# Kernel optimization log

Hardware: AMD Instinct MI355X
Metric: run time of the kernel (lower is better)

The kernel has to match this reference:

```python
import jax, jax.numpy as jnp
import numpy as np

L, B, D = 2048, 8, 2048


def setup_inputs() -> dict:
    key = jax.random.key(0)
    k1, k2, k3 = jax.random.split(key, 3)
    x = jax.random.normal(k1, (L, B, D), dtype=jnp.float32)
    x_mix_last = jnp.zeros((B, D), dtype=jnp.float32)
    factor_param = jax.random.uniform(k2, (D,), dtype=jnp.float32)
    W = jax.random.normal(k3, (D, D), dtype=jnp.float32) * (1.0 / np.sqrt(D))
    return {"x": x, "x_mix_last": x_mix_last, "factor_param": factor_param, "W": W}


def reference(x, x_mix_last, factor_param, W):
    seq_len = x.shape[0]
    factor = jax.nn.sigmoid(factor_param)                      # [D]
    t = jnp.arange(seq_len, dtype=x.dtype)[:, None]            # [L,1]
    factor_progression = jnp.power(factor[None, :], t)         # [L,D] = factor**t
    # FFT-based causal convolution: y[t] = sum_{s<=t} factor**(t-s) * x[s]
    n = 2 * seq_len
    fft_fp = jnp.fft.rfft(factor_progression, n=n, axis=0)     # [L+1, D]
    fft_x = jnp.fft.rfft(x, n=n, axis=0)                       # [L+1, B, D]
    conv = jnp.fft.irfft(fft_x * fft_fp[:, None, :], axis=0)[:seq_len]  # [L,B,D]
    conv = conv.astype(x.dtype)
    # EMA mix: carried state decays as factor**(t+1); new input weighted by (1-factor)
    x_mix = (x_mix_last[None, :, :] * factor_progression[:, None, :] * factor
             + (1.0 - factor) * conv)                          # [L,B,D]
    # Linear mixing W (no bias): out = x_mix @ W.T
    return jnp.einsum('lbd,ed->lbe', x_mix, W)
```

## Files before the change

### kernel.cpp

```cpp
#include <hip/hip_runtime.h>
#include <hip/hip_bf16.h>
#include <stdint.h>

#define L_SEQ 2048
#define BATCH 8
#define DIM   2048
#define M_DIM (L_SEQ * BATCH)
#define N_DIM DIM
#define K_DIM DIM

typedef short bf16x8 __attribute__((ext_vector_type(8)));
typedef float f32x4  __attribute__((ext_vector_type(4)));
typedef unsigned short u16x4 __attribute__((ext_vector_type(4)));

__device__ inline unsigned short f2bf_rn(float f) {
    unsigned int u = __float_as_uint(f);
    u += 0x7FFF + ((u >> 16) & 1);
    return (unsigned short)(u >> 16);
}

__device__ inline void gload16(const void* g, void* l) {
    __builtin_amdgcn_global_load_lds(
        (const __attribute__((address_space(1))) void*)g,
        (__attribute__((address_space(3))) void*)l, 16, 0, 0);
}

__global__ void cvt_w_kernel(const float* __restrict__ W,
                             unsigned short* __restrict__ Wb) {
    int i = blockIdx.x * 256 + threadIdx.x;
    const float4 v = *reinterpret_cast<const float4*>(W + (size_t)i * 4);
    u16x4 r;
    r.x = f2bf_rn(v.x); r.y = f2bf_rn(v.y);
    r.z = f2bf_rn(v.z); r.w = f2bf_rn(v.w);
    *reinterpret_cast<u16x4*>(Wb + (size_t)i * 4) = r;
}

#define SCH 128
#define SLB 64
__global__ void ema_scan_kernel(const float* __restrict__ x,
                                const float* __restrict__ xml,
                                const float* __restrict__ fparam,
                                unsigned short* __restrict__ xm) {
    int g  = blockIdx.x * 256 + threadIdx.x;
    int dp = (g & 1023) * 2;
    int b  = (g >> 10) & (BATCH - 1);
    int ch = g >> 13;

    float2 pv = *reinterpret_cast<const float2*>(fparam + dp);
    const float f0 = 1.0f / (1.0f + expf(-pv.x));
    const float f1 = 1.0f / (1.0f + expf(-pv.y));
    float2 xlv = *reinterpret_cast<const float2*>(xml + b * DIM + dp);
    const float om0 = 1.0f - f0, om1 = 1.0f - f1;

    const int t0 = ch * SCH;
    int ts = t0 - SLB; if (ts < 0) ts = 0;
    const int stride2 = (BATCH * DIM) / 2;

    const float2* xp = reinterpret_cast<const float2*>(x) +
                       (size_t)ts * stride2 + (b * DIM + dp) / 2;
    float c0 = 0.0f, c1 = 0.0f;
    #pragma unroll 8
    for (int t = ts; t < t0; ++t) {
        float2 v = *xp;
        c0 = fmaf(c0, f0, v.x);
        c1 = fmaf(c1, f1, v.y);
        xp += stride2;
    }
    float pw0 = powf(f0, (float)(t0 + 1));
    float pw1 = powf(f1, (float)(t0 + 1));
    ushort2* op = reinterpret_cast<ushort2*>(xm + (size_t)t0 * BATCH * DIM + b * DIM + dp);
    #pragma unroll 8
    for (int k = 0; k < SCH; ++k) {
        float2 v = *xp;
        c0 = fmaf(c0, f0, v.x);
        c1 = fmaf(c1, f1, v.y);
        ushort2 r;
        r.x = f2bf_rn(fmaf(xlv.x, pw0, om0 * c0));
        r.y = f2bf_rn(fmaf(xlv.y, pw1, om1 * c1));
        *op = r;
        pw0 *= f0; pw1 *= f1;
        xp += stride2; op += stride2;
    }
}

#define NT_K (K_DIM / 64)
#define NI   (NT_K / 2)

__global__ void __launch_bounds__(512, 2)
gemm8_kernel(const unsigned short* __restrict__ A,
             const unsigned short* __restrict__ Bt,
             float* __restrict__ C) {
    extern __shared__ __attribute__((aligned(16))) char smem[];

    int bid = blockIdx.x;
    int swz = (bid & 7) * 64 + (bid >> 3);
    const int tm = swz >> 3;
    const int tn = swz & 7;

    const int tid  = threadIdx.x;
    const int lane = tid & 63;
    const int w    = tid >> 6;
    const int wr   = w >> 2;
    const int wn   = w & 3;

    const int aoff0 = (tid >> 3) * (K_DIM * 2) + (((tid & 7) ^ ((tid >> 3) & 7)) * 16);
    const int aoff1 = aoff0 + 64 * (K_DIM * 2);
    const char* gAc = (const char*)(A  + (size_t)tm * 256 * K_DIM);
    const char* gBc = (const char*)(Bt + (size_t)tn * 256 * K_DIM);

#define STAGE_A(bs, ha, t) do {                                              \
        const char* _s = gAc + (size_t)((ha) * 128) * (K_DIM * 2) + (size_t)(t) * 128; \
        char* _d = smem + (bs) * 65536 + (ha) * 16384 + tid * 16;            \
        gload16(_s + aoff0, _d);                                             \
        gload16(_s + aoff1, _d + 8192);                                      \
    } while (0)
#define STAGE_B(bs, hb, t) do {                                              \
        const char* _s = gBc + (size_t)((hb) * 128) * (K_DIM * 2) + (size_t)(t) * 128; \
        char* _d = smem + (bs) * 65536 + 32768 + (hb) * 16384 + tid * 16;    \
        gload16(_s + aoff0, _d);                                             \
        gload16(_s + aoff1, _d + 8192);                                      \
    } while (0)

    const int ra   = wr * 64 + (lane & 15);
    const int rb   = wn * 32 + (lane & 15);
    const int khi  = (lane >> 4) * 16;
    const int cxor = (lane & 7) << 4;

    f32x4 acc[8][4];
    #pragma unroll
    for (int m = 0; m < 8; ++m)
        #pragma unroll
        for (int n = 0; n < 4; ++n)
            acc[m][n] = (f32x4){0.f, 0.f, 0.f, 0.f};

    bf16x8 afr[4][2];
    bf16x8 bfr[2][2];

#define LOAD_A(qa, bs) do {                                                  \
        const char* _ab = smem + (bs) * 65536;                               \
        _Pragma("unroll") for (int m = 0; m < 4; ++m) {                      \
            int _r = (qa) * 128 + ra + m * 16;                               \
            _Pragma("unroll") for (int ks = 0; ks < 2; ++ks)                 \
                afr[m][ks] = *(const bf16x8*)(_ab + _r * 128 +               \
                                              ((ks * 64 + khi) ^ cxor));     \
        }                                                                    \
    } while (0)
#define LOAD_B(qb, bs) do {                                                  \
        const char* _bb = smem + (bs) * 65536 + 32768;                       \
        _Pragma("unroll") for (int n = 0; n < 2; ++n) {                      \
            int _rn = (qb) * 128 + rb + n * 16;                              \
            _Pragma("unroll") for (int ks = 0; ks < 2; ++ks)                 \
                bfr[n][ks] = *(const bf16x8*)(_bb + _rn * 128 +              \
                                              ((ks * 64 + khi) ^ cxor));     \
        }                                                                    \
    } while (0)

#define PHASE_MFMA(qa, qb, VN, ...) do {                                     \
        __VA_ARGS__;                                                         \
        __builtin_amdgcn_s_barrier();                                        \
        __builtin_amdgcn_s_setprio(1);                                       \
        _Pragma("unroll") for (int m = 0; m < 4; ++m)                        \
            _Pragma("unroll") for (int n = 0; n < 2; ++n)                    \
                _Pragma("unroll") for (int ks = 0; ks < 2; ++ks)             \
                    acc[(qa) * 4 + m][(qb) * 2 + n] =                        \
                        __builtin_amdgcn_mfma_f32_16x16x32_bf16(             \
                            afr[m][ks], bfr[n][ks],                          \
                            acc[(qa) * 4 + m][(qb) * 2 + n], 0, 0, 0);       \
        __builtin_amdgcn_s_setprio(0);                                       \
        asm volatile("s_waitcnt vmcnt(" #VN ")" ::: "memory");               \
        __builtin_amdgcn_s_barrier();                                        \
    } while (0)

#define GROUP(bs, S1, S2, S3, S4, V1, V2, V3, V4) do {                       \
        LOAD_A(0, bs); LOAD_B(0, bs);                                        \
        PHASE_MFMA(0, 0, V1, S1);                                            \
        LOAD_B(1, bs);                                                       \
        PHASE_MFMA(0, 1, V2, S2);                                            \
        LOAD_A(1, bs);                                                       \
        PHASE_MFMA(1, 1, V3, S3);                                            \
        LOAD_B(0, bs);                                                       \
        PHASE_MFMA(1, 0, V4, S4);                                            \
    } while (0)

    STAGE_A(0, 0, 0); STAGE_B(0, 0, 0); STAGE_B(0, 1, 0); STAGE_A(0, 1, 0);
    asm volatile("s_waitcnt vmcnt(4)" ::: "memory");
    __builtin_amdgcn_s_barrier();

    for (int i = 0; i < NI - 1; ++i) {
        const int t1 = 2 * i + 1, t2 = 2 * i + 2;
        GROUP(0, STAGE_A(1, 0, t1), STAGE_B(1, 0, t1),
                 STAGE_B(1, 1, t1), STAGE_A(1, 1, t1), 4, 4, 4, 4);
        GROUP(1, STAGE_A(0, 0, t2), STAGE_B(0, 0, t2),
                 STAGE_B(0, 1, t2), STAGE_A(0, 1, t2), 4, 4, 4, 4);
    }
    GROUP(0, STAGE_A(1, 0, NT_K - 1), STAGE_B(1, 0, NT_K - 1),
             STAGE_B(1, 1, NT_K - 1), STAGE_A(1, 1, NT_K - 1), 4, 4, 4, 4);
    GROUP(1, (void)0, (void)0, (void)0, (void)0, 2, 0, 0, 0);

    float* Cb = C + (size_t)(tm * 256) * N_DIM + tn * 256;
    const int col0 = lane & 15;
    const int rg   = (lane >> 4) * 4;
    #pragma unroll
    for (int qa2 = 0; qa2 < 2; ++qa2)
        #pragma unroll
        for (int m = 0; m < 4; ++m)
            #pragma unroll
            for (int j = 0; j < 4; ++j) {
                int row = qa2 * 128 + wr * 64 + m * 16 + rg + j;
                float* rp = Cb + (size_t)row * N_DIM;
                #pragma unroll
                for (int qb2 = 0; qb2 < 2; ++qb2)
                    #pragma unroll
                    for (int n = 0; n < 2; ++n)
                        rp[qb2 * 128 + wn * 32 + n * 16 + col0] =
                            acc[qa2 * 4 + m][qb2 * 2 + n][j];
            }
#undef GROUP
#undef PHASE_MFMA
#undef LOAD_A
#undef LOAD_B
#undef STAGE_A
#undef STAGE_B
}

extern "C" void kernel_launch(void* const* d_in, const int* in_sizes, int n_in,
                              void* d_out, int out_size, void* d_ws, size_t ws_size,
                              hipStream_t stream) {
    const float* x   = (const float*)d_in[0];
    const float* xml = (const float*)d_in[1];
    const float* fp  = (const float*)d_in[2];
    const float* W   = (const float*)d_in[3];
    float* out = (float*)d_out;

    unsigned short* xmix = (unsigned short*)d_ws;
    unsigned short* wb   = xmix + (size_t)M_DIM * K_DIM;

    (void)hipFuncSetAttribute(reinterpret_cast<const void*>(&gemm8_kernel),
                              hipFuncAttributeMaxDynamicSharedMemorySize, 131072);

    cvt_w_kernel<<<4096, 256, 0, stream>>>(W, wb);
    ema_scan_kernel<<<512, 256, 0, stream>>>(x, xml, fp, xmix);
    gemm8_kernel<<<(M_DIM / 256) * (N_DIM / 256), 512, 131072, stream>>>(xmix, wb, out);
}
```

Measured before the change: 363.0 us.

## Restructure GEMM main loop into two phases with double B fragment registers

Each k-group of the bf16 MFMA GEMM now runs as two phases instead of four. Both B quadrant fragments are held in separate register arrays, so each A-row phase issues 32 MFMAs against both B halves. This halves the barriers and waitcnt points per group and avoids reloading the B fragments. The stage loads are redistributed unevenly (three stages, then one) with adjusted vmcnt thresholds. In exchange it uses more VGPRs and gives coarser overlap of global-to-LDS loads with compute.

```diff
diff --git a/kernel.cpp b/kernel.cpp
--- a/kernel.cpp
+++ b/kernel.cpp
@@ -122,7 +122,7 @@
     } while (0)
 
     const int ra   = wr * 64 + (lane & 15);
-    const int rb   = wn * 32 + (lane & 15);
+    const int rbB  = wn * 32 + (lane & 15);
     const int khi  = (lane >> 4) * 16;
     const int cxor = (lane & 7) << 4;
 
@@ -134,7 +134,8 @@
             acc[m][n] = (f32x4){0.f, 0.f, 0.f, 0.f};
 
     bf16x8 afr[4][2];
-    bf16x8 bfr[2][2];
+    bf16x8 bfr0[2][2];
+    bf16x8 bfr1[2][2];
 
 #define LOAD_A(qa, bs) do {                                                  \
         const char* _ab = smem + (bs) * 65536;                               \
@@ -145,57 +146,66 @@
                                               ((ks * 64 + khi) ^ cxor));     \
         }                                                                    \
     } while (0)
-#define LOAD_B(qb, bs) do {                                                  \
+#define LOAD_B(qb, dst, bs) do {                                             \
         const char* _bb = smem + (bs) * 65536 + 32768;                       \
         _Pragma("unroll") for (int n = 0; n < 2; ++n) {                      \
-            int _rn = (qb) * 128 + rb + n * 16;                              \
+            int _rn = (qb) * 128 + rbB + n * 16;                             \
             _Pragma("unroll") for (int ks = 0; ks < 2; ++ks)                 \
-                bfr[n][ks] = *(const bf16x8*)(_bb + _rn * 128 +              \
+                dst[n][ks] = *(const bf16x8*)(_bb + _rn * 128 +              \
                                               ((ks * 64 + khi) ^ cxor));     \
         }                                                                    \
     } while (0)
 
-#define PHASE_MFMA(qa, qb, VN, ...) do {                                     \
-        __VA_ARGS__;                                                         \
+#define MFMA_ROW(qa)                                                         \
+        _Pragma("unroll") for (int m = 0; m < 4; ++m)                        \
+            _Pragma("unroll") for (int n = 0; n < 2; ++n)                    \
+                _Pragma("unroll") for (int ks = 0; ks < 2; ++ks) {           \
+                    acc[(qa) * 4 + m][n] =                                   \
+                        __builtin_amdgcn_mfma_f32_16x16x32_bf16(             \
+                            afr[m][ks], bfr0[n][ks],                         \
+                            acc[(qa) * 4 + m][n], 0, 0, 0);                  \
+                    acc[(qa) * 4 + m][2 + n] =                               \
+                        __builtin_amdgcn_mfma_f32_16x16x32_bf16(             \
+                            afr[m][ks], bfr1[n][ks],                         \
+                            acc[(qa) * 4 + m][2 + n], 0, 0, 0);              \
+                }
+
+#define PHASE_END(VN)                                                        \
+        asm volatile("s_waitcnt vmcnt(" #VN ")" ::: "memory");               \
+        __builtin_amdgcn_s_barrier();
+
+#define GROUP(bs, SA, SB, VA, VB) do {                                       \
+        LOAD_A(0, bs); LOAD_B(0, bfr0, bs); LOAD_B(1, bfr1, bs);             \
+        SA;                                                                  \
         __builtin_amdgcn_s_barrier();                                        \
         __builtin_amdgcn_s_setprio(1);                                       \
-        _Pragma("unroll") for (int m = 0; m < 4; ++m)                        \
-            _Pragma("unroll") for (int n = 0; n < 2; ++n)                    \
-                _Pragma("unroll") for (int ks = 0; ks < 2; ++ks)             \
-                    acc[(qa) * 4 + m][(qb) * 2 + n] =                        \
-                        __builtin_amdgcn_mfma_f32_16x16x32_bf16(             \
-                            afr[m][ks], bfr[n][ks],                          \
-                            acc[(qa) * 4 + m][(qb) * 2 + n], 0, 0, 0);       \
+        MFMA_ROW(0)                                                          \
         __builtin_amdgcn_s_setprio(0);                                       \
-        asm volatile("s_waitcnt vmcnt(" #VN ")" ::: "memory");               \
+        PHASE_END(VA)                                                        \
+        LOAD_A(1, bs);                                                       \
+        SB;                                                                  \
         __builtin_amdgcn_s_barrier();                                        \
-    } while (0)
-
-#define GROUP(bs, S1, S2, S3, S4, V1, V2, V3, V4) do {                       \
-        LOAD_A(0, bs); LOAD_B(0, bs);                                        \
-        PHASE_MFMA(0, 0, V1, S1);                                            \
-        LOAD_B(1, bs);                                                       \
-        PHASE_MFMA(0, 1, V2, S2);                                            \
-        LOAD_A(1, bs);                                                       \
-        PHASE_MFMA(1, 1, V3, S3);                                            \
-        LOAD_B(0, bs);                                                       \
-        PHASE_MFMA(1, 0, V4, S4);                                            \
+        __builtin_amdgcn_s_setprio(1);                                       \
+        MFMA_ROW(1)                                                          \
+        __builtin_amdgcn_s_setprio(0);                                       \
+        PHASE_END(VB)                                                        \
     } while (0)
 
     STAGE_A(0, 0, 0); STAGE_B(0, 0, 0); STAGE_B(0, 1, 0); STAGE_A(0, 1, 0);
-    asm volatile("s_waitcnt vmcnt(4)" ::: "memory");
+    asm volatile("s_waitcnt vmcnt(2)" ::: "memory");
     __builtin_amdgcn_s_barrier();
 
     for (int i = 0; i < NI - 1; ++i) {
         const int t1 = 2 * i + 1, t2 = 2 * i + 2;
-        GROUP(0, STAGE_A(1, 0, t1), STAGE_B(1, 0, t1),
-                 STAGE_B(1, 1, t1), STAGE_A(1, 1, t1), 4, 4, 4, 4);
-        GROUP(1, STAGE_A(0, 0, t2), STAGE_B(0, 0, t2),
-                 STAGE_B(0, 1, t2), STAGE_A(0, 1, t2), 4, 4, 4, 4);
+        GROUP(0, { STAGE_A(1, 0, t1); STAGE_B(1, 0, t1); STAGE_B(1, 1, t1); },
+                 { STAGE_A(1, 1, t1); }, 6, 2);
+        GROUP(1, { STAGE_A(0, 0, t2); STAGE_B(0, 0, t2); STAGE_B(0, 1, t2); },
+                 { STAGE_A(0, 1, t2); }, 6, 2);
     }
-    GROUP(0, STAGE_A(1, 0, NT_K - 1), STAGE_B(1, 0, NT_K - 1),
-             STAGE_B(1, 1, NT_K - 1), STAGE_A(1, 1, NT_K - 1), 4, 4, 4, 4);
-    GROUP(1, (void)0, (void)0, (void)0, (void)0, 2, 0, 0, 0);
+    GROUP(0, { STAGE_A(1, 0, NT_K - 1); STAGE_B(1, 0, NT_K - 1);
+               STAGE_B(1, 1, NT_K - 1); },
+             { STAGE_A(1, 1, NT_K - 1); }, 6, 2);
+    GROUP(1, (void)0, (void)0, 0, 0);
 
     float* Cb = C + (size_t)(tm * 256) * N_DIM + tn * 256;
     const int col0 = lane & 15;
@@ -216,7 +226,8 @@
                             acc[qa2 * 4 + m][qb2 * 2 + n][j];
             }
 #undef GROUP
-#undef PHASE_MFMA
+#undef PHASE_END
+#undef MFMA_ROW
 #undef LOAD_A
 #undef LOAD_B
 #undef STAGE_A
```

New measurement: 360.5 us. No clear change (-0.7%).
